# Kernel tuning notes

Hardware: AMD Instinct MI355X
Metric: run time of the kernel (lower is better)

Reference implementation:

```python
import jax, jax.numpy as jnp
import numpy as np


def setup_inputs() -> dict:
    key = jax.random.key(0)
    B, S, N, D = 4, 512, 8, 256
    ks = jax.random.split(key, 5)
    s = 0.02
    inp = {"x": jax.random.normal(ks[0], (B, S, N, D), jnp.float32)}
    for k, name in zip(ks[1:], ["Wq", "Wk", "Wv", "Wo"]):
        inp[name] = jax.random.normal(k, (D, D), jnp.float32) * s
    for name in ["bq", "bk", "bv", "bo"]:
        inp[name] = jnp.zeros((D,), jnp.float32)
    inp["gamma"] = jnp.ones((D,), jnp.float32)
    inp["beta"] = jnp.zeros((D,), jnp.float32)
    inp["num_heads"] = 8
    return inp


def reference(x, Wq, bq, Wk, bk, Wv, bv, Wo, bo, gamma, beta, num_heads):
    B, S, N, D = x.shape
    H = num_heads
    hd = D // H
    # sinusoidal positional encoding: even dims sin, odd dims cos
    pos = jnp.arange(S, dtype=jnp.float32)[:, None]                      # (S,1)
    div = jnp.exp(jnp.arange(0, D, 2, dtype=jnp.float32) * (-np.log(10000.0) / D))
    ang = pos * div                                                       # (S, D/2)
    pe = jnp.stack([jnp.sin(ang), jnp.cos(ang)], axis=-1).reshape(S, D)   # (S, D)
    x_pos = x + pe[None, :, None, :]                                      # (B,S,N,D)
    # fold sensors into batch: (B*N, S, D)
    xr = x_pos.transpose(0, 2, 1, 3).reshape(B * N, S, D)

    def proj(W, b):
        y = xr @ W.T + b                                                  # torch Linear
        return y.reshape(B * N, S, H, hd).transpose(0, 2, 1, 3)          # (BN,H,S,hd)

    Q, K, V = proj(Wq, bq), proj(Wk, bk), proj(Wv, bv)
    scores = jnp.einsum('bhqd,bhkd->bhqk', Q, K) / np.sqrt(hd)            # (BN,H,S,S)
    causal = jnp.tril(jnp.ones((S, S), dtype=bool))
    scores = jnp.where(causal[None, None], scores, jnp.float32(-1e9))
    attn = jax.nn.softmax(scores, axis=-1)                                # dropout = eval mode
    out = jnp.einsum('bhqk,bhkd->bhqd', attn, V)                          # (BN,H,S,hd)
    out = out.transpose(0, 2, 1, 3).reshape(B * N, S, D)
    out = out @ Wo.T + bo
    out = out.reshape(B, N, S, D).transpose(0, 2, 1, 3)                   # (B,S,N,D)
    y = out + x
    mu = jnp.mean(y, axis=-1, keepdims=True)
    var = jnp.var(y, axis=-1, keepdims=True)
    return (y - mu) / jnp.sqrt(var + 1e-5) * gamma + beta
```

## Files before the change

kernel.cpp:

```cpp
#include <hip/hip_runtime.h>
#include <hip/hip_bf16.h>
#include <math.h>

#define B_   4
#define S_   512
#define N_   8
#define D_   256
#define H_   8
#define HD_  32
#define BN_  32
#define MTOT (BN_ * S_)

typedef __attribute__((ext_vector_type(8))) short short8;
typedef __attribute__((ext_vector_type(4))) short short4v;
typedef __attribute__((ext_vector_type(4))) float floatx4;

#define QSCALE 0.25503468f

__device__ __forceinline__ unsigned short f2bf(float f) {
    union { float f; unsigned u; } c; c.f = f;
    unsigned lsb = (c.u >> 16) & 1u;
    c.u += 0x7fffu + lsb;
    return (unsigned short)(c.u >> 16);
}
__device__ __forceinline__ unsigned short f2bf_ru(float f) {
    union { float f; unsigned u; } c; c.f = f;
    return (unsigned short)((c.u + 0x8000u) >> 16);
}
__device__ __forceinline__ float fexp2(float x) {
    float r; asm("v_exp_f32 %0, %1" : "=v"(r) : "v"(x)); return r;
}

__global__ __launch_bounds__(256) void prep_kernel(const float* __restrict__ x,
                                                   const float* __restrict__ Wq,
                                                   const float* __restrict__ Wk,
                                                   const float* __restrict__ Wv,
                                                   const float* __restrict__ Wo,
                                                   unsigned short* __restrict__ xpos,
                                                   unsigned short* __restrict__ wdst) {
    int bid = blockIdx.x;
    if (bid < 4096) {
        int idx4 = bid * 256 + threadIdx.x;
        int d0 = (idx4 << 2) & (D_ - 1);
        int s  = (idx4 >> 6) & (S_ - 1);
        int bn = idx4 >> 15;
        int b = bn >> 3, n = bn & 7;
        floatx4 xv = *(const floatx4*)(x + ((((size_t)b * S_ + s) * N_ + n) << 8) + d0);
        const float cfreq = -9.210340371976184f / 256.0f;
        float f0 = __expf((float)d0 * cfreq);
        float f1 = __expf((float)(d0 + 2) * cfreq);
        float a0 = (float)s * f0, a1 = (float)s * f1;
        short4v o;
        o[0] = (short)f2bf(xv[0] + __sinf(a0));
        o[1] = (short)f2bf(xv[1] + __cosf(a0));
        o[2] = (short)f2bf(xv[2] + __sinf(a1));
        o[3] = (short)f2bf(xv[3] + __cosf(a1));
        *(short4v*)(xpos + ((size_t)idx4 << 2)) = o;
    } else {
        int idx = (bid - 4096) * 256 + threadIdx.x;
        int which = idx >> 16, off = idx & 65535;
        const float* W = (which == 0) ? Wq : (which == 1) ? Wk : (which == 2) ? Wv : Wo;
        wdst[idx] = f2bf(W[off]);
    }
}

__global__ __launch_bounds__(256) void gemm_qkv_kernel(const unsigned short* __restrict__ A,
                                                       const unsigned short* __restrict__ W,
                                                       const float* __restrict__ bq,
                                                       const float* __restrict__ bk,
                                                       const float* __restrict__ bv,
                                                       unsigned short* __restrict__ Qh,
                                                       unsigned short* __restrict__ Kh,
                                                       unsigned short* __restrict__ Vt) {
    int wv = threadIdx.x >> 6, lane = threadIdx.x & 63;
    int col = lane & 15, quad = lane >> 4;
    int m_w = blockIdx.x * 128 + (wv >> 1) * 64;
    int n_w = blockIdx.y * 128 + (wv & 1) * 64;

    const short8* Ap = (const short8*)(A + (size_t)(m_w + col) * 256 + quad * 8);
    const short8* Bp = (const short8*)(W + (size_t)(n_w + col) * 256 + quad * 8);

    floatx4 acc[4][4] = {};
#pragma unroll
    for (int kk = 0; kk < 8; ++kk) {
        short8 a[4], b[4];
#pragma unroll
        for (int t = 0; t < 4; ++t) {
            a[t] = Ap[t * 512 + kk * 4];
            b[t] = Bp[t * 512 + kk * 4];
        }
#pragma unroll
        for (int mt = 0; mt < 4; ++mt)
#pragma unroll
            for (int nt = 0; nt < 4; ++nt)
                acc[mt][nt] = __builtin_amdgcn_mfma_f32_16x16x32_bf16(a[mt], b[nt], acc[mt][nt], 0, 0, 0);
    }

    int sel = blockIdx.y >> 1;
    const float* bias = (sel == 0) ? bq : (sel == 1) ? bk : bv;
#pragma unroll
    for (int nt = 0; nt < 4; ++nt) {
        int c = n_w + nt * 16 + col - sel * 256;
        float bv_ = bias[c];
#pragma unroll
        for (int mt = 0; mt < 4; ++mt) {
            int m0 = m_w + mt * 16 + quad * 4;
            int bn = m0 >> 9, s0 = m0 & (S_ - 1);
            if (sel == 2) {
                short4v pack;
#pragma unroll
                for (int r = 0; r < 4; ++r) pack[r] = (short)f2bf(acc[mt][nt][r] + bv_);
                *(short4v*)(Vt + (((size_t)((bn << 8) + c)) << 9) + s0) = pack;
            } else {
                int h2 = c >> 5, dl = c & 31;
                unsigned short* dst = ((sel == 0) ? Qh : Kh)
                    + ((((size_t)(bn * 8 + h2)) * 512 + s0) << 5) + dl;
                if (sel == 0) {
#pragma unroll
                    for (int r = 0; r < 4; ++r)
                        dst[r << 5] = f2bf((acc[mt][nt][r] + bv_) * QSCALE);
                } else {
#pragma unroll
                    for (int r = 0; r < 4; ++r)
                        dst[r << 5] = f2bf(acc[mt][nt][r] + bv_);
                }
            }
        }
    }
}

#define PSTR  40
#define KSTR  40
#define VSTR  520
__global__ __launch_bounds__(1024) void fattn_kernel(const unsigned short* __restrict__ Qh,
                                                     const unsigned short* __restrict__ Kh,
                                                     const unsigned short* __restrict__ Vt,
                                                     unsigned short* __restrict__ O) {
    __shared__ unsigned short Klds[S_ * KSTR];
    __shared__ unsigned short Vlds[HD_ * VSTR];
    __shared__ unsigned short Plds[16][16 * PSTR];

    int t = threadIdx.x;
    int bnh = blockIdx.x;
    int bn = bnh >> 3, h = bnh & 7;

    const unsigned short* Ksrc = Kh + ((size_t)bnh << 14);
    const unsigned short* Vsrc = Vt + (((size_t)bnh * HD_) << 9);
#pragma unroll
    for (int i = 0; i < 2; ++i) {
        int c = t + i * 1024;
        int kr = c >> 2, ks = c & 3;
        *(short8*)&Klds[kr * KSTR + ks * 8] = *(const short8*)(Ksrc + kr * 32 + ks * 8);
        int vr = c >> 6, vs = c & 63;
        *(short8*)&Vlds[vr * VSTR + vs * 8] = *(const short8*)(Vsrc + vr * 512 + vs * 8);
    }
    __syncthreads();

    int wv = t >> 6, lane = t & 63;
    int col = lane & 15, quad = lane >> 4;
    unsigned short* P = &Plds[wv][0];
    int qts[2] = { wv, 31 - wv };

#pragma unroll
    for (int ui = 0; ui < 2; ++ui) {
        int q0 = qts[ui] * 16;
        short8 qfrag = *(const short8*)(Qh + (((size_t)(bnh * S_ + q0 + col)) << 5) + quad * 8);
        float l = 0.f;
        floatx4 o0 = {0.f, 0.f, 0.f, 0.f};
        floatx4 o1 = {0.f, 0.f, 0.f, 0.f};
        int lastk = q0 >> 5;

        for (int kt = 0; kt <= lastk; ++kt) {
            int k0 = kt * 32;
            short8 kf0 = *(const short8*)&Klds[(k0 + col) * KSTR + quad * 8];
            short8 kf1 = *(const short8*)&Klds[(k0 + 16 + col) * KSTR + quad * 8];
            floatx4 z = {0.f, 0.f, 0.f, 0.f};
            floatx4 st0 = __builtin_amdgcn_mfma_f32_16x16x32_bf16(kf0, qfrag, z, 0, 0, 0);
            floatx4 st1 = __builtin_amdgcn_mfma_f32_16x16x32_bf16(kf1, qfrag, z, 0, 0, 0);

            if (kt == lastk) {
                int qg = q0 + col;
#pragma unroll
                for (int r = 0; r < 4; ++r) {
                    if (k0 + quad * 4 + r > qg)      st0[r] = -1e30f;
                    if (k0 + 16 + quad * 4 + r > qg) st1[r] = -1e30f;
                }
            }

            float p[8]; float ts = 0.f;
#pragma unroll
            for (int r = 0; r < 4; ++r) {
                p[r]     = fexp2(st0[r]);
                p[4 + r] = fexp2(st1[r]);
                ts += p[r] + p[4 + r];
            }
            ts += __shfl_xor(ts, 16);
            ts += __shfl_xor(ts, 32);
            l += ts;

            short4v pk0, pk1;
#pragma unroll
            for (int r = 0; r < 4; ++r) {
                pk0[r] = (short)f2bf_ru(p[r]);
                pk1[r] = (short)f2bf_ru(p[4 + r]);
            }
            *(short4v*)&P[col * PSTR + quad * 4]      = pk0;
            *(short4v*)&P[col * PSTR + 16 + quad * 4] = pk1;
            asm volatile("s_waitcnt lgkmcnt(0)" ::: "memory");
            short8 pfrag = *(const short8*)&P[col * PSTR + quad * 8];

            short8 vf0 = *(const short8*)&Vlds[col * VSTR + k0 + quad * 8];
            short8 vf1 = *(const short8*)&Vlds[(16 + col) * VSTR + k0 + quad * 8];
            o0 = __builtin_amdgcn_mfma_f32_16x16x32_bf16(vf0, pfrag, o0, 0, 0, 0);
            o1 = __builtin_amdgcn_mfma_f32_16x16x32_bf16(vf1, pfrag, o1, 0, 0, 0);
        }

        float inv = 1.0f / l;
        unsigned short* Op = O + (((size_t)(bn * S_ + q0 + col)) << 8) + h * HD_;
        short4v s0v, s1v;
#pragma unroll
        for (int r = 0; r < 4; ++r) {
            s0v[r] = (short)f2bf(o0[r] * inv);
            s1v[r] = (short)f2bf(o1[r] * inv);
        }
        *(short4v*)(Op + quad * 4)      = s0v;
        *(short4v*)(Op + 16 + quad * 4) = s1v;
    }
}

__global__ __launch_bounds__(256) void gemm_o_ln_kernel(const unsigned short* __restrict__ A,
                                                        const unsigned short* __restrict__ W,
                                                        const float* __restrict__ bo,
                                                        const float* __restrict__ x,
                                                        const float* __restrict__ gamma,
                                                        const float* __restrict__ beta,
                                                        float* __restrict__ out) {
    __shared__ float lsum[4][64];
    __shared__ float lss[4][64];
    __shared__ float lmu[64];
    __shared__ float lrs[64];

    int wv = threadIdx.x >> 6, lane = threadIdx.x & 63;
    int col = lane & 15, quad = lane >> 4;
    int m_b = blockIdx.x * 64;
    int n_w = wv * 64;

    const short8* Ap = (const short8*)(A + (size_t)(m_b + col) * 256 + quad * 8);
    const short8* Bp = (const short8*)(W + (size_t)(n_w + col) * 256 + quad * 8);

    floatx4 acc[4][4] = {};
#pragma unroll
    for (int kk = 0; kk < 8; ++kk) {
        short8 a[4], b[4];
#pragma unroll
        for (int t = 0; t < 4; ++t) {
            a[t] = Ap[t * 512 + kk * 4];
            b[t] = Bp[t * 512 + kk * 4];
        }
#pragma unroll
        for (int mt = 0; mt < 4; ++mt)
#pragma unroll
            for (int nt = 0; nt < 4; ++nt)
                acc[mt][nt] = __builtin_amdgcn_mfma_f32_16x16x32_bf16(a[mt], b[nt], acc[mt][nt], 0, 0, 0);
    }

    int bn = m_b >> 9, s0 = m_b & (S_ - 1);
    int b_ = bn >> 3, n_ = bn & 7;
    const float* xrow = x + ((((size_t)b_ * S_ + s0) * N_ + n_) << 8);
    float* orow = out + ((((size_t)b_ * S_ + s0) * N_ + n_) << 8);

    float psum[4][4] = {};
    float pss[4][4]  = {};
#pragma unroll
    for (int nt = 0; nt < 4; ++nt) {
        int c = n_w + nt * 16 + col;
        float bv_ = bo[c];
#pragma unroll
        for (int mt = 0; mt < 4; ++mt) {
            int sl = mt * 16 + quad * 4;
#pragma unroll
            for (int r = 0; r < 4; ++r) {
                float y = acc[mt][nt][r] + bv_ + xrow[(size_t)(sl + r) * 2048 + c];
                acc[mt][nt][r] = y;
                psum[mt][r] += y;
                pss[mt][r]  += y * y;
            }
        }
    }
#pragma unroll
    for (int off = 8; off >= 1; off >>= 1) {
#pragma unroll
        for (int mt = 0; mt < 4; ++mt)
#pragma unroll
            for (int r = 0; r < 4; ++r) {
                psum[mt][r] += __shfl_xor(psum[mt][r], off);
                pss[mt][r]  += __shfl_xor(pss[mt][r], off);
            }
    }
    if (col == 0) {
#pragma unroll
        for (int mt = 0; mt < 4; ++mt)
#pragma unroll
            for (int r = 0; r < 4; ++r) {
                lsum[wv][mt * 16 + quad * 4 + r] = psum[mt][r];
                lss[wv][mt * 16 + quad * 4 + r]  = pss[mt][r];
            }
    }
    __syncthreads();
    if (threadIdx.x < 64) {
        int row = threadIdx.x;
        float s  = lsum[0][row] + lsum[1][row] + lsum[2][row] + lsum[3][row];
        float ss = lss[0][row] + lss[1][row] + lss[2][row] + lss[3][row];
        float mu = s * (1.0f / 256.0f);
        float var = ss * (1.0f / 256.0f) - mu * mu;
        lmu[row] = mu;
        lrs[row] = rsqrtf(var + 1e-5f);
    }
    __syncthreads();

#pragma unroll
    for (int nt = 0; nt < 4; ++nt) {
        int c = n_w + nt * 16 + col;
        float g  = gamma[c];
        float be = beta[c];
#pragma unroll
        for (int mt = 0; mt < 4; ++mt) {
            int sl = mt * 16 + quad * 4;
#pragma unroll
            for (int r = 0; r < 4; ++r)
                orow[(size_t)(sl + r) * 2048 + c] =
                    (acc[mt][nt][r] - lmu[sl + r]) * lrs[sl + r] * g + be;
        }
    }
}

extern "C" void kernel_launch(void* const* d_in, const int* in_sizes, int n_in,
                              void* d_out, int out_size, void* d_ws, size_t ws_size,
                              hipStream_t stream) {
    const float* x     = (const float*)d_in[0];
    const float* Wq    = (const float*)d_in[1];
    const float* Wk    = (const float*)d_in[2];
    const float* Wv    = (const float*)d_in[3];
    const float* Wo    = (const float*)d_in[4];
    const float* bq    = (const float*)d_in[5];
    const float* bk    = (const float*)d_in[6];
    const float* bv    = (const float*)d_in[7];
    const float* bo    = (const float*)d_in[8];
    const float* gamma = (const float*)d_in[9];
    const float* beta  = (const float*)d_in[10];

    char* w = (char*)d_ws;
    const size_t SZ = (size_t)MTOT * D_ * 2;
    unsigned short* xpos = (unsigned short*)(w);
    unsigned short* Qh   = (unsigned short*)(w + SZ);
    unsigned short* Kh   = (unsigned short*)(w + 2 * SZ);
    unsigned short* Vt   = (unsigned short*)(w + 3 * SZ);
    unsigned short* Ab   = (unsigned short*)(w + 4 * SZ);
    unsigned short* Wbf  = (unsigned short*)(w + 5 * SZ);

    prep_kernel<<<5120, 256, 0, stream>>>(x, Wq, Wk, Wv, Wo, xpos, Wbf);
    gemm_qkv_kernel<<<dim3(128, 6), 256, 0, stream>>>(xpos, Wbf, bq, bk, bv, Qh, Kh, Vt);
    fattn_kernel<<<256, 1024, 0, stream>>>(Qh, Kh, Vt, Ab);
    gemm_o_ln_kernel<<<256, 256, 0, stream>>>(Ab, Wbf + 3 * 65536, bo, x, gamma, beta, (float*)d_out);
}
```

Baseline: 149.7 us.

## Store K/V/P in fragment-linear LDS layout and prefetch Q fragments

Rearranges K and V in shared memory so that each MFMA fragment is a contiguous 64-lane block, read with a lane-linear address instead of padded strided rows. P is also stored in fragment order, and the explicit s_waitcnt before reading P back is removed. Q fragments for both query tiles are loaded before the K/V staging so that global latency overlaps. The aim is to cut LDS bank conflicts and address arithmetic in the inner loop. Dropping the explicit wait relies on the compiler to order the P store and load correctly.

```diff
diff --git a/kernel.cpp b/kernel.cpp
--- a/kernel.cpp
+++ b/kernel.cpp
@@ -129,42 +129,46 @@
     }
 }
 
-#define PSTR  40
-#define KSTR  40
-#define VSTR  520
 __global__ __launch_bounds__(1024) void fattn_kernel(const unsigned short* __restrict__ Qh,
                                                      const unsigned short* __restrict__ Kh,
                                                      const unsigned short* __restrict__ Vt,
                                                      unsigned short* __restrict__ O) {
-    __shared__ unsigned short Klds[S_ * KSTR];
-    __shared__ unsigned short Vlds[HD_ * VSTR];
-    __shared__ unsigned short Plds[16][16 * PSTR];
+    __shared__ unsigned short Klds[16384];
+    __shared__ unsigned short Vlds[16384];
+    __shared__ unsigned short Plds[16][512];
 
     int t = threadIdx.x;
     int bnh = blockIdx.x;
     int bn = bnh >> 3, h = bnh & 7;
-
-    const unsigned short* Ksrc = Kh + ((size_t)bnh << 14);
-    const unsigned short* Vsrc = Vt + (((size_t)bnh * HD_) << 9);
-#pragma unroll
-    for (int i = 0; i < 2; ++i) {
-        int c = t + i * 1024;
-        int kr = c >> 2, ks = c & 3;
-        *(short8*)&Klds[kr * KSTR + ks * 8] = *(const short8*)(Ksrc + kr * 32 + ks * 8);
-        int vr = c >> 6, vs = c & 63;
-        *(short8*)&Vlds[vr * VSTR + vs * 8] = *(const short8*)(Vsrc + vr * 512 + vs * 8);
-    }
-    __syncthreads();
-
     int wv = t >> 6, lane = t & 63;
     int col = lane & 15, quad = lane >> 4;
     unsigned short* P = &Plds[wv][0];
     int qts[2] = { wv, 31 - wv };
 
+    short8 qf[2];
+#pragma unroll
+    for (int ui = 0; ui < 2; ++ui)
+        qf[ui] = *(const short8*)(Qh + (((size_t)(bnh * S_ + qts[ui] * 16 + col)) << 5) + quad * 8);
+
+    const unsigned short* Ksrc = Kh + ((size_t)bnh << 14);
+    const unsigned short* Vsrc = Vt + ((size_t)bnh << 14);
+#pragma unroll
+    for (int i = 0; i < 2; ++i) {
+        int g = t + i * 1024;
+        int kt = g >> 7, r = g & 127;
+        int half = r >> 6, lin = r & 63;
+        int c = lin & 15, q = lin >> 4;
+        *(short8*)&Klds[(kt << 10) + (half << 9) + (lin << 3)] =
+            *(const short8*)(Ksrc + ((kt * 32 + half * 16 + c) << 5) + (q << 3));
+        *(short8*)&Vlds[(kt << 10) + (half << 9) + (lin << 3)] =
+            *(const short8*)(Vsrc + (((half << 4) + c) << 9) + (kt << 5) + (q << 3));
+    }
+    __syncthreads();
+
 #pragma unroll
     for (int ui = 0; ui < 2; ++ui) {
         int q0 = qts[ui] * 16;
-        short8 qfrag = *(const short8*)(Qh + (((size_t)(bnh * S_ + q0 + col)) << 5) + quad * 8);
+        short8 qfrag = qf[ui];
         float l = 0.f;
         floatx4 o0 = {0.f, 0.f, 0.f, 0.f};
         floatx4 o1 = {0.f, 0.f, 0.f, 0.f};
@@ -172,8 +176,9 @@
 
         for (int kt = 0; kt <= lastk; ++kt) {
             int k0 = kt * 32;
-            short8 kf0 = *(const short8*)&Klds[(k0 + col) * KSTR + quad * 8];
-            short8 kf1 = *(const short8*)&Klds[(k0 + 16 + col) * KSTR + quad * 8];
+            int tb = kt << 10;
+            short8 kf0 = *(const short8*)&Klds[tb + (lane << 3)];
+            short8 kf1 = *(const short8*)&Klds[tb + 512 + (lane << 3)];
             floatx4 z = {0.f, 0.f, 0.f, 0.f};
             floatx4 st0 = __builtin_amdgcn_mfma_f32_16x16x32_bf16(kf0, qfrag, z, 0, 0, 0);
             floatx4 st1 = __builtin_amdgcn_mfma_f32_16x16x32_bf16(kf1, qfrag, z, 0, 0, 0);
@@ -204,13 +209,13 @@
                 pk0[r] = (short)f2bf_ru(p[r]);
                 pk1[r] = (short)f2bf_ru(p[4 + r]);
             }
-            *(short4v*)&P[col * PSTR + quad * 4]      = pk0;
-            *(short4v*)&P[col * PSTR + 16 + quad * 4] = pk1;
-            asm volatile("s_waitcnt lgkmcnt(0)" ::: "memory");
-            short8 pfrag = *(const short8*)&P[col * PSTR + quad * 8];
-
-            short8 vf0 = *(const short8*)&Vlds[col * VSTR + k0 + quad * 8];
-            short8 vf1 = *(const short8*)&Vlds[(16 + col) * VSTR + k0 + quad * 8];
+            int qh_ = quad >> 1, ql_ = (quad & 1) << 2;
+            *(short4v*)&P[(((qh_) * 16 + col) << 3) + ql_]     = pk0;
+            *(short4v*)&P[(((2 + qh_) * 16 + col) << 3) + ql_] = pk1;
+            short8 pfrag = *(const short8*)&P[lane << 3];
+
+            short8 vf0 = *(const short8*)&Vlds[tb + (lane << 3)];
+            short8 vf1 = *(const short8*)&Vlds[tb + 512 + (lane << 3)];
             o0 = __builtin_amdgcn_mfma_f32_16x16x32_bf16(vf0, pfrag, o0, 0, 0, 0);
             o1 = __builtin_amdgcn_mfma_f32_16x16x32_bf16(vf1, pfrag, o1, 0, 0, 0);
         }
```

Result: no change. 148.4 us (-0.9%).
